# Kernel optimization log

Measured on AMD Instinct MI355X. Metric: run time of the kernel, lower is better.

The kernel has to match this reference:

```python
import jax, jax.numpy as jnp
import numpy as np

N_CARD, N_TX, N_MER = 100_000, 1_000_000, 10_000
E = 1_000_000
H = 128


def setup_inputs() -> dict:
    key = jax.random.key(0)
    ks = iter(jax.random.split(key, 32))
    nrm = lambda shape, s=1.0: jax.random.normal(next(ks), shape, jnp.float32) * s
    W = 0.05  # weight scale for numerical sanity across two relu layers
    inp = {
        "x_card": nrm((N_CARD, 32)),
        "x_tx": nrm((N_TX, 64)),
        "x_mer": nrm((N_MER, 32)),
        # layer-1 SAGEConv params per edge type: lin_l (src->H, w/ bias), lin_r (dst->H)
        "l1_pays_wl": nrm((32, H), W), "l1_pays_bl": nrm((H,), W), "l1_pays_wr": nrm((64, H), W),
        "l1_recv_wl": nrm((32, H), W), "l1_recv_bl": nrm((H,), W), "l1_recv_wr": nrm((64, H), W),
        "l1_rpays_wl": nrm((64, H), W), "l1_rpays_bl": nrm((H,), W), "l1_rpays_wr": nrm((32, H), W),
        "l1_rrecv_wl": nrm((64, H), W), "l1_rrecv_bl": nrm((H,), W), "l1_rrecv_wr": nrm((32, H), W),
        # layer-2: all relations are H->H; stacked in order [pays, receives, rev_pays, rev_receives]
        "w2l": nrm((4, H, H), W), "b2": nrm((4, H), W), "w2r": nrm((4, H, H), W),
        # final lazy Linear(-1, out_channels=1) -> (H, 1)
        "wf": nrm((H, 1), W), "bf": nrm((1,), W),
        "pays_src": jax.random.randint(next(ks), (E,), 0, N_CARD, jnp.int32),
        "pays_dst": jnp.arange(E, dtype=jnp.int32),
        "recv_src": jax.random.randint(next(ks), (E,), 0, N_MER, jnp.int32),
        "recv_dst": jnp.arange(E, dtype=jnp.int32),
    }
    return inp


def _sage(x_src, x_dst, src, dst, wl, bl, wr, n_dst):
    """PyG SAGEConv(aggr='mean'): lin_l(mean_j x_j) + lin_r(x_root)."""
    msg = x_src[src]  # [E, d_src] gather
    s = jax.ops.segment_sum(msg, dst, num_segments=n_dst)
    cnt = jax.ops.segment_sum(jnp.ones((src.shape[0], 1), msg.dtype), dst, num_segments=n_dst)
    mean = s / jnp.maximum(cnt, 1.0)
    return mean @ wl + bl + x_dst @ wr


def reference(x_card, x_tx, x_mer,
              l1_pays_wl, l1_pays_bl, l1_pays_wr,
              l1_recv_wl, l1_recv_bl, l1_recv_wr,
              l1_rpays_wl, l1_rpays_bl, l1_rpays_wr,
              l1_rrecv_wl, l1_rrecv_bl, l1_rrecv_wr,
              w2l, b2, w2r, wf, bf,
              pays_src, pays_dst, recv_src, recv_dst):
    # ---- layer 1 (HeteroConv aggr='sum' over relations sharing a dst type) ----
    tx = (_sage(x_card, x_tx, pays_src, pays_dst, l1_pays_wl, l1_pays_bl, l1_pays_wr, N_TX)
          + _sage(x_mer, x_tx, recv_src, recv_dst, l1_recv_wl, l1_recv_bl, l1_recv_wr, N_TX))
    # rev_pays / rev_receives are the transposed edge lists
    card = _sage(x_tx, x_card, pays_dst, pays_src, l1_rpays_wl, l1_rpays_bl, l1_rpays_wr, N_CARD)
    mer = _sage(x_tx, x_mer, recv_dst, recv_src, l1_rrecv_wl, l1_rrecv_bl, l1_rrecv_wr, N_MER)
    tx, card, mer = jax.nn.relu(tx), jax.nn.relu(card), jax.nn.relu(mer)
    # ---- layer 2 (only transaction output feeds the head; card/mer layer-2 outputs unused) ----
    tx2 = (_sage(card, tx, pays_src, pays_dst, w2l[0], b2[0], w2r[0], N_TX)
           + _sage(mer, tx, recv_src, recv_dst, w2l[1], b2[1], w2r[1], N_TX))
    tx2 = jax.nn.relu(tx2)
    return tx2 @ wf + bf  # [N_TX, 1]
```

## Files before the change

### kernel.cpp

```cpp
#include <hip/hip_runtime.h>
#include <hip/hip_bf16.h>
#include <stdint.h>

#define NCARD 100000
#define NTX   1000000
#define NMER  10000
#define NE    1000000
#define CAPC  48
#define CAPM  192
#define NCB   3125
#define NMB   313


typedef __attribute__((ext_vector_type(8))) short bf16x8;
typedef __attribute__((ext_vector_type(4))) float f32x4;

__device__ inline unsigned short f2bf(float f) {
  union { float f; uint32_t u; } v; v.f = f;
  uint32_t r = v.u + 0x7FFF + ((v.u >> 16) & 1);
  return (unsigned short)(r >> 16);
}
__device__ inline float bf2f(unsigned short u) {
  union { uint32_t u; float f; } v; v.u = ((uint32_t)u) << 16;
  return v.f;
}
__device__ inline uint32_t addpack2(uint32_t a, uint32_t b) {
  float lo = bf2f((unsigned short)(a & 0xffff)) + bf2f((unsigned short)(b & 0xffff));
  float hi = bf2f((unsigned short)(a >> 16))   + bf2f((unsigned short)(b >> 16));
  return (uint32_t)f2bf(lo) | ((uint32_t)f2bf(hi) << 16);
}

#define OFF_WR1T  0u
#define OFF_W2RT  4096u
#define OFF_B1    12288u
#define OFF_B2    12416u
#define OFF_CW1   12544u
#define OFF_CW2   18688u
#define OFF_CW3   26880u
#define OFF_MW1   28928u
#define OFF_MW2   35072u
#define OFF_MW3   43264u
#define OFF_CQ    45312u
#define OFF_MQ    12845312u
#define OFF_CCNT  14125312u
#define OFF_MCNT  14225312u
#define OFF_CBUK  14235312u
#define OFF_MBUK  19035312u
#define OFF_XB    20955312u
#define WS_END    52955312u

__global__ __launch_bounds__(256) void k_prep_all(
    const float* __restrict__ pays_wr, const float* __restrict__ recv_wr,
    const float* __restrict__ w2r, const float* __restrict__ pays_bl,
    const float* __restrict__ recv_bl, const float* __restrict__ b2,
    unsigned short* __restrict__ wr1t, unsigned short* __restrict__ w2rt,
    float* __restrict__ b1sum, float* __restrict__ b2sum,
    const float* __restrict__ c_wl64, const float* __restrict__ c_wr32,
    const float* __restrict__ c_w2, const float* __restrict__ c_wg,
    unsigned short* __restrict__ cw1, unsigned short* __restrict__ cw2,
    unsigned short* __restrict__ cw3,
    const float* __restrict__ m_wl64, const float* __restrict__ m_wr32,
    const float* __restrict__ m_w2, const float* __restrict__ m_wg,
    unsigned short* __restrict__ mw1, unsigned short* __restrict__ mw2,
    unsigned short* __restrict__ mw3)
{
  const int grp = blockIdx.x >> 6;
  const int i = (blockIdx.x & 63) * 256 + threadIdx.x;
  if (grp == 0) {
    if (i < 8192) {
      int n = i >> 6, k = i & 63;
      wr1t[i] = f2bf(pays_wr[k * 128 + n] + recv_wr[k * 128 + n]);
    }
    if (i < 16384) {
      int n = i >> 7, k = i & 127;
      w2rt[i] = f2bf(w2r[k * 128 + n] + w2r[16384 + k * 128 + n]);
    }
    if (i < 128) {
      b1sum[i] = pays_bl[i] + recv_bl[i];
      b2sum[i] = b2[i] + b2[128 + i];
    }
  } else {
    const float* wl64 = (grp == 1) ? c_wl64 : m_wl64;
    const float* wr32 = (grp == 1) ? c_wr32 : m_wr32;
    const float* w2   = (grp == 1) ? c_w2   : m_w2;
    const float* wg   = (grp == 1) ? c_wg   : m_wg;
    unsigned short* w1t = (grp == 1) ? cw1 : mw1;
    unsigned short* w2t = (grp == 1) ? cw2 : mw2;
    unsigned short* w3t = (grp == 1) ? cw3 : mw3;
    if (i < 12288) {
      int n = i / 96, k = i % 96;
      float v = (k < 64) ? wl64[k * 128 + n] : wr32[(k - 64) * 128 + n];
      w1t[i] = f2bf(v);
    }
    if (i < 16384) { int n = i >> 7, k = i & 127; w2t[i] = f2bf(w2[k * 128 + n]); }
    if (i < 4096)  { int n = i >> 5, k = i & 31;  w3t[i] = f2bf(wg[k * 128 + n]); }
  }
}

__global__ __launch_bounds__(256) void k_convert_build(
    const float* __restrict__ x, unsigned short* __restrict__ xb,
    const int* __restrict__ ps, const int* __restrict__ rs,
    int* __restrict__ ccnt, int* __restrict__ mcnt,
    int* __restrict__ cbuk, int* __restrict__ mbuk)
{
  int64_t i = (int64_t)blockIdx.x * 256 + threadIdx.x;
  if (i < 16000000) {
    float4 v = ((const float4*)x)[i];
    unsigned short p[4] = { f2bf(v.x), f2bf(v.y), f2bf(v.z), f2bf(v.w) };
    *(uint2*)&xb[i * 4] = *(const uint2*)p;
  }
  if (i < NE) {
    int e = (int)i;
    int c = ps[e];
    int pos = atomicAdd(ccnt + c, 1);
    if (pos < CAPC) cbuk[c * CAPC + pos] = e;
    int m = rs[e];
    int pm = atomicAdd(mcnt + m, 1);
    if (pm < CAPM) mbuk[m * CAPM + pm] = e;
  }
}

__global__ __launch_bounds__(256) void k_node_both(
    const int* __restrict__ ccnt, const int* __restrict__ cbuk,
    const int* __restrict__ mcnt, const int* __restrict__ mbuk,
    const unsigned short* __restrict__ xb,
    const float* __restrict__ x_card, const float* __restrict__ x_mer,
    const unsigned short* __restrict__ cw1, const unsigned short* __restrict__ cw2,
    const unsigned short* __restrict__ cw3, const float* __restrict__ cbl,
    const unsigned short* __restrict__ mw1, const unsigned short* __restrict__ mw2,
    const unsigned short* __restrict__ mw3, const float* __restrict__ mbl,
    const float* __restrict__ b1sum, const float* __restrict__ b2sum,
    unsigned short* __restrict__ cq, unsigned short* __restrict__ mq)
{
  const bool iscard = blockIdx.x < NCB;
  const int* cnt = iscard ? ccnt : mcnt;
  const int* buk = iscard ? cbuk : mbuk;
  const int cap  = iscard ? CAPC : CAPM;
  const int R    = iscard ? NCARD : NMER;
  const float* x_node = iscard ? x_card : x_mer;
  const unsigned short* w1t = iscard ? cw1 : mw1;
  const unsigned short* w2t = iscard ? cw2 : mw2;
  const unsigned short* w3t = iscard ? cw3 : mw3;
  const float* bl = iscard ? cbl : mbl;
  unsigned short* q = iscard ? cq : mq;
  const int n0 = (iscard ? blockIdx.x : blockIdx.x - NCB) * 32;

  __shared__ unsigned short ms[32 * 64];
  __shared__ unsigned short xs2[32 * 32];
  __shared__ unsigned short ts[32 * 128];
  __shared__ float bll[128], ba1[128], ba2[128];
  const int tid = threadIdx.x;
  const int wv = tid >> 6, l = tid & 63;
  const int lr = l & 15, lk = l >> 4;

  bf16x8 f1[2][3], f2w[2][4], f3[2];
#pragma unroll
  for (int c = 0; c < 2; ++c) {
    const int n = wv * 32 + c * 16 + lr;
#pragma unroll
    for (int k = 0; k < 3; ++k)
      f1[c][k] = *(const bf16x8*)(w1t + n * 96 + k * 32 + lk * 8);
#pragma unroll
    for (int k = 0; k < 4; ++k)
      f2w[c][k] = *(const bf16x8*)(w2t + n * 128 + k * 32 + lk * 8);
    f3[c] = *(const bf16x8*)(w3t + n * 32 + lk * 8);
  }
  if (tid < 128) {
    bll[tid] = bl[tid];
    ba1[tid] = iscard ? b1sum[tid] : 0.f;
    ba2[tid] = iscard ? b2sum[tid] : 0.f;
  }

  const int half = l >> 5, c32 = l & 31;
  for (int rr = wv; rr < 32; rr += 4) {
    const int node = n0 + rr;
    int deg = 0;
    if (node < R) deg = cnt[node];
    const int64_t base = (int64_t)node * cap;
    float a0 = 0.f, a1 = 0.f;
    int p = half;
    for (; p + 14 < deg; p += 16) {
      int ei[8];
      uint32_t vi[8];
#pragma unroll
      for (int u = 0; u < 8; ++u) ei[u] = buk[base + p + 2 * u];
#pragma unroll
      for (int u = 0; u < 8; ++u)
        vi[u] = *(const uint32_t*)&xb[(int64_t)ei[u] * 64 + c32 * 2];
#pragma unroll
      for (int u = 0; u < 8; ++u) {
        a0 += bf2f((unsigned short)(vi[u] & 0xffff));
        a1 += bf2f((unsigned short)(vi[u] >> 16));
      }
    }
    for (; p + 6 < deg; p += 8) {
      int e0 = buk[base + p],     e1 = buk[base + p + 2];
      int e2 = buk[base + p + 4], e3 = buk[base + p + 6];
      uint32_t v0 = *(const uint32_t*)&xb[(int64_t)e0 * 64 + c32 * 2];
      uint32_t v1 = *(const uint32_t*)&xb[(int64_t)e1 * 64 + c32 * 2];
      uint32_t v2 = *(const uint32_t*)&xb[(int64_t)e2 * 64 + c32 * 2];
      uint32_t v3 = *(const uint32_t*)&xb[(int64_t)e3 * 64 + c32 * 2];
      a0 += bf2f((unsigned short)(v0 & 0xffff)) + bf2f((unsigned short)(v1 & 0xffff))
          + bf2f((unsigned short)(v2 & 0xffff)) + bf2f((unsigned short)(v3 & 0xffff));
      a1 += bf2f((unsigned short)(v0 >> 16)) + bf2f((unsigned short)(v1 >> 16))
          + bf2f((unsigned short)(v2 >> 16)) + bf2f((unsigned short)(v3 >> 16));
    }
    for (; p < deg; p += 2) {
      int e = buk[base + p];
      uint32_t v = *(const uint32_t*)&xb[(int64_t)e * 64 + c32 * 2];
      a0 += bf2f((unsigned short)(v & 0xffff));
      a1 += bf2f((unsigned short)(v >> 16));
    }
    a0 += __shfl_xor(a0, 32, 64);
    a1 += __shfl_xor(a1, 32, 64);
    if (half == 0) {
      float inv = 1.f / fmaxf((float)deg, 1.f);
      unsigned short pr[2] = { f2bf(a0 * inv), f2bf(a1 * inv) };
      int li = (rr * 64 + c32 * 2) ^ ((rr & 7) << 3);
      *(uint32_t*)&ms[li] = *(const uint32_t*)pr;
    }
  }
#pragma unroll
  for (int q4 = 0; q4 < 4; ++q4) {
    int id = q4 * 256 + tid;
    int r = id >> 5, c = id & 31;
    float v = (n0 + r < R) ? x_node[(int64_t)(n0 + r) * 32 + c] : 0.f;
    xs2[(r * 32 + c) ^ ((r & 3) << 3)] = f2bf(v);
  }
  __syncthreads();

#pragma unroll
  for (int rt = 0; rt < 2; ++rt) {
    const int arow = rt * 16 + lr;
    const int sw = (arow & 7) << 3, sw2 = (arow & 3) << 3;
    bf16x8 a0 = *(const bf16x8*)&ms[(arow * 64 + 0  + lk * 8) ^ sw];
    bf16x8 a1 = *(const bf16x8*)&ms[(arow * 64 + 32 + lk * 8) ^ sw];
    bf16x8 ax = *(const bf16x8*)&xs2[(arow * 32 + lk * 8) ^ sw2];
    f32x4 acc0 = {0.f,0.f,0.f,0.f}, acc1 = {0.f,0.f,0.f,0.f};
    acc0 = __builtin_amdgcn_mfma_f32_16x16x32_bf16(a0, f1[0][0], acc0, 0, 0, 0);
    acc0 = __builtin_amdgcn_mfma_f32_16x16x32_bf16(a1, f1[0][1], acc0, 0, 0, 0);
    acc0 = __builtin_amdgcn_mfma_f32_16x16x32_bf16(ax, f1[0][2], acc0, 0, 0, 0);
    acc1 = __builtin_amdgcn_mfma_f32_16x16x32_bf16(a0, f1[1][0], acc1, 0, 0, 0);
    acc1 = __builtin_amdgcn_mfma_f32_16x16x32_bf16(a1, f1[1][1], acc1, 0, 0, 0);
    acc1 = __builtin_amdgcn_mfma_f32_16x16x32_bf16(ax, f1[1][2], acc1, 0, 0, 0);
#pragma unroll
    for (int c = 0; c < 2; ++c) {
      const int col = wv * 32 + c * 16 + lr;
#pragma unroll
      for (int i = 0; i < 4; ++i) {
        const int r = rt * 16 + lk * 4 + i;
        float v = (c ? acc1[i] : acc0[i]) + bll[col];
        ts[(r * 128 + col) ^ ((r & 7) << 3)] = f2bf(fmaxf(v, 0.f));
      }
    }
  }
  __syncthreads();

#pragma unroll
  for (int rt = 0; rt < 2; ++rt) {
    const int arow = rt * 16 + lr;
    const int sw = (arow & 7) << 3, sw2 = (arow & 3) << 3;
    f32x4 b0 = {0.f,0.f,0.f,0.f}, b1a = {0.f,0.f,0.f,0.f};
#pragma unroll
    for (int kk = 0; kk < 4; ++kk) {
      bf16x8 a = *(const bf16x8*)&ts[(arow * 128 + kk * 32 + lk * 8) ^ sw];
      b0  = __builtin_amdgcn_mfma_f32_16x16x32_bf16(a, f2w[0][kk], b0, 0, 0, 0);
      b1a = __builtin_amdgcn_mfma_f32_16x16x32_bf16(a, f2w[1][kk], b1a, 0, 0, 0);
    }
    bf16x8 ax = *(const bf16x8*)&xs2[(arow * 32 + lk * 8) ^ sw2];
    f32x4 g0 = {0.f,0.f,0.f,0.f}, g1a = {0.f,0.f,0.f,0.f};
    g0  = __builtin_amdgcn_mfma_f32_16x16x32_bf16(ax, f3[0], g0, 0, 0, 0);
    g1a = __builtin_amdgcn_mfma_f32_16x16x32_bf16(ax, f3[1], g1a, 0, 0, 0);
#pragma unroll
    for (int c = 0; c < 2; ++c) {
#pragma unroll
      for (int i = 0; i < 4; ++i) {
        const int node = n0 + rt * 16 + lk * 4 + i;
        const int col = wv * 32 + c * 16 + lr;
        if (node < R) {
          q[node * 256 + col]       = f2bf((c ? g1a[i] : g0[i]) + ba1[col]);
          q[node * 256 + 128 + col] = f2bf((c ? b1a[i] : b0[i]) + ba2[col]);
        }
      }
    }
  }
}

#define TXR 32
__global__ __launch_bounds__(256) void k_fused_tx_mfma(
    const unsigned short* __restrict__ xb,
    const int* __restrict__ ps, const int* __restrict__ rs,
    const unsigned short* __restrict__ cq, const unsigned short* __restrict__ mq,
    const unsigned short* __restrict__ wr1t, const unsigned short* __restrict__ w2rt,
    const float* __restrict__ wf, const float* __restrict__ bfp,
    float* __restrict__ out)
{
  __shared__ unsigned short xs[TXR * 64];
  __shared__ unsigned short ts[TXR * 128];
  __shared__ unsigned short g1[TXR * 128];
  __shared__ unsigned short g2[TXR * 128];
  __shared__ float partial[4][TXR];
  __shared__ float wfl[128];

  const int tid = threadIdx.x;
  const int wv = tid >> 6;
  const int l  = tid & 63;
  const int lr = l & 15;
  const int lk = l >> 4;

  bf16x8 w1f[2][2], w2f[2][4];
#pragma unroll
  for (int c = 0; c < 2; ++c) {
    const int n = (wv * 2 + c) * 16 + lr;
#pragma unroll
    for (int kk = 0; kk < 2; ++kk)
      w1f[c][kk] = *(const bf16x8*)(wr1t + n * 64 + kk * 32 + lk * 8);
#pragma unroll
    for (int kk = 0; kk < 4; ++kk)
      w2f[c][kk] = *(const bf16x8*)(w2rt + n * 128 + kk * 32 + lk * 8);
  }
  if (tid < 128) wfl[tid] = wf[tid];
  const float bfv = bfp[0];

  const uint32_t* cqd = (const uint32_t*)cq;
  const uint32_t* mqd = (const uint32_t*)mq;

  const int r_x = tid >> 3, seg_x = tid & 7;
  const int64_t stride = (int64_t)gridDim.x * TXR;
  int64_t row0 = (int64_t)blockIdx.x * TXR;

  uint4 xv;
  uint32_t rc1[8], rm1[8], rc2[8], rm2[8];

  if (row0 < NTX) {
    xv = *(const uint4*)&xb[(row0 + r_x) * 64 + seg_x * 8];
#pragma unroll
    for (int p = 0; p < 8; ++p) {
      const int r = p * 4 + wv;
      const int64_t c = ps[row0 + r];
      const int64_t m = rs[row0 + r];
      rc1[p] = cqd[c * 128 + l];      rm1[p] = mqd[m * 128 + l];
      rc2[p] = cqd[c * 128 + 64 + l]; rm2[p] = mqd[m * 128 + 64 + l];
    }
  }

  for (; row0 < NTX; row0 += stride) {
    __syncthreads();
    *(uint4*)&xs[(r_x * 64 + seg_x * 8) ^ ((r_x & 7) << 3)] = xv;
#pragma unroll
    for (int p = 0; p < 8; ++p) {
      const int r = p * 4 + wv;
      const int dst = r * 64 + (l ^ (p << 3));
      ((uint32_t*)g1)[dst] = addpack2(rc1[p], rm1[p]);
      ((uint32_t*)g2)[dst] = addpack2(rc2[p], rm2[p]);
    }
    __syncthreads();

    const int64_t nxt = row0 + stride;
    if (nxt < NTX) {
      xv = *(const uint4*)&xb[(nxt + r_x) * 64 + seg_x * 8];
#pragma unroll
      for (int p = 0; p < 8; ++p) {
        const int r = p * 4 + wv;
        const int64_t c = ps[nxt + r];
        const int64_t m = rs[nxt + r];
        rc1[p] = cqd[c * 128 + l];      rm1[p] = mqd[m * 128 + l];
        rc2[p] = cqd[c * 128 + 64 + l]; rm2[p] = mqd[m * 128 + 64 + l];
      }
    }

#pragma unroll
    for (int rt = 0; rt < 2; ++rt) {
      const int arow = rt * 16 + lr;
      const int sw = (arow & 7) << 3;
      bf16x8 a0  = *(const bf16x8*)&xs[(arow * 64 + 0  + lk * 8) ^ sw];
      bf16x8 a1v = *(const bf16x8*)&xs[(arow * 64 + 32 + lk * 8) ^ sw];
      f32x4 acc0 = {0.f,0.f,0.f,0.f}, acc1 = {0.f,0.f,0.f,0.f};
      acc0 = __builtin_amdgcn_mfma_f32_16x16x32_bf16(a0,  w1f[0][0], acc0, 0, 0, 0);
      acc0 = __builtin_amdgcn_mfma_f32_16x16x32_bf16(a1v, w1f[0][1], acc0, 0, 0, 0);
      acc1 = __builtin_amdgcn_mfma_f32_16x16x32_bf16(a0,  w1f[1][0], acc1, 0, 0, 0);
      acc1 = __builtin_amdgcn_mfma_f32_16x16x32_bf16(a1v, w1f[1][1], acc1, 0, 0, 0);
      const int gx = (rt * 4 + lk) << 3;
#pragma unroll
      for (int c = 0; c < 2; ++c) {
        const int col = wv * 32 + c * 16 + lr;
        const int gofs = (((col >> 1) ^ gx) << 1) + (col & 1);
        const f32x4 acc = c ? acc1 : acc0;
#pragma unroll
        for (int i = 0; i < 4; ++i) {
          const int r = rt * 16 + lk * 4 + i;
          float v = acc[i] + bf2f(g1[r * 128 + gofs]);
          ts[(r * 128 + col) ^ ((r & 7) << 3)] = f2bf(fmaxf(v, 0.f));
        }
      }
    }
    __syncthreads();

#pragma unroll
    for (int rt = 0; rt < 2; ++rt) {
      const int arow = rt * 16 + lr;
      const int sw = (arow & 7) << 3;
      f32x4 acc0 = {0.f,0.f,0.f,0.f}, acc1 = {0.f,0.f,0.f,0.f};
#pragma unroll
      for (int kk = 0; kk < 4; ++kk) {
        bf16x8 a = *(const bf16x8*)&ts[(arow * 128 + kk * 32 + lk * 8) ^ sw];
        acc0 = __builtin_amdgcn_mfma_f32_16x16x32_bf16(a, w2f[0][kk], acc0, 0, 0, 0);
        acc1 = __builtin_amdgcn_mfma_f32_16x16x32_bf16(a, w2f[1][kk], acc1, 0, 0, 0);
      }
      const int gx = (rt * 4 + lk) << 3;
#pragma unroll
      for (int i = 0; i < 4; ++i) {
        const int r = rt * 16 + lk * 4 + i;
        float sum = 0.f;
#pragma unroll
        for (int c = 0; c < 2; ++c) {
          const int col = wv * 32 + c * 16 + lr;
          const int gofs = (((col >> 1) ^ gx) << 1) + (col & 1);
          float y = (c ? acc1[i] : acc0[i]) + bf2f(g2[r * 128 + gofs]);
          sum = fmaf(fmaxf(y, 0.f), wfl[col], sum);
        }
#pragma unroll
        for (int off = 1; off < 16; off <<= 1) sum += __shfl_xor(sum, off, 64);
        if (lr == 0) partial[wv][r] = sum;
      }
    }
    __syncthreads();
    if (tid < TXR)
      out[row0 + tid] = partial[0][tid] + partial[1][tid] + partial[2][tid]
                      + partial[3][tid] + bfv;
  }
}

extern "C" void kernel_launch(void* const* d_in, const int* in_sizes, int n_in,
                              void* d_out, int out_size, void* d_ws, size_t ws_size,
                              hipStream_t stream) {
  const float* x_card = (const float*)d_in[0];
  const float* x_tx   = (const float*)d_in[1];
  const float* x_mer  = (const float*)d_in[2];
  const float* l1_pays_wl = (const float*)d_in[3];
  const float* l1_pays_bl = (const float*)d_in[4];
  const float* l1_pays_wr = (const float*)d_in[5];
  const float* l1_recv_wl = (const float*)d_in[6];
  const float* l1_recv_bl = (const float*)d_in[7];
  const float* l1_recv_wr = (const float*)d_in[8];
  const float* l1_rpays_wl = (const float*)d_in[9];
  const float* l1_rpays_bl = (const float*)d_in[10];
  const float* l1_rpays_wr = (const float*)d_in[11];
  const float* l1_rrecv_wl = (const float*)d_in[12];
  const float* l1_rrecv_bl = (const float*)d_in[13];
  const float* l1_rrecv_wr = (const float*)d_in[14];
  const float* w2l = (const float*)d_in[15];
  const float* b2  = (const float*)d_in[16];
  const float* w2r = (const float*)d_in[17];
  const float* wf  = (const float*)d_in[18];
  const float* bf  = (const float*)d_in[19];
  const int* pays_src = (const int*)d_in[20];
  const int* recv_src = (const int*)d_in[22];

  float* ws = (float*)d_ws;
  unsigned short* wr1t = (unsigned short*)(ws + OFF_WR1T);
  unsigned short* w2rt = (unsigned short*)(ws + OFF_W2RT);
  float* b1sum = ws + OFF_B1;
  float* b2sum = ws + OFF_B2;
  unsigned short* cw1 = (unsigned short*)(ws + OFF_CW1);
  unsigned short* cw2 = (unsigned short*)(ws + OFF_CW2);
  unsigned short* cw3 = (unsigned short*)(ws + OFF_CW3);
  unsigned short* mw1 = (unsigned short*)(ws + OFF_MW1);
  unsigned short* mw2 = (unsigned short*)(ws + OFF_MW2);
  unsigned short* mw3 = (unsigned short*)(ws + OFF_MW3);
  unsigned short* cq  = (unsigned short*)(ws + OFF_CQ);
  unsigned short* mq  = (unsigned short*)(ws + OFF_MQ);
  int* ccnt = (int*)(ws + OFF_CCNT);
  int* mcnt = (int*)(ws + OFF_MCNT);
  int* cbuk = (int*)(ws + OFF_CBUK);
  int* mbuk = (int*)(ws + OFF_MBUK);
  unsigned short* xb = (unsigned short*)(ws + OFF_XB);

  hipMemsetAsync((char*)d_ws + (size_t)OFF_CCNT * 4, 0,
                 (size_t)(OFF_CBUK - OFF_CCNT) * 4, stream);

  k_prep_all<<<192, 256, 0, stream>>>(
      l1_pays_wr, l1_recv_wr, w2r, l1_pays_bl, l1_recv_bl, b2,
      wr1t, w2rt, b1sum, b2sum,
      l1_rpays_wl, l1_rpays_wr, w2l, l1_pays_wl, cw1, cw2, cw3,
      l1_rrecv_wl, l1_rrecv_wr, w2l + 16384, l1_recv_wl, mw1, mw2, mw3);

  k_convert_build<<<62500, 256, 0, stream>>>(x_tx, xb, pays_src, recv_src,
                                             ccnt, mcnt, cbuk, mbuk);

  k_node_both<<<NCB + NMB, 256, 0, stream>>>(
      ccnt, cbuk, mcnt, mbuk, xb, x_card, x_mer,
      cw1, cw2, cw3, l1_rpays_bl,
      mw1, mw2, mw3, l1_rrecv_bl,
      b1sum, b2sum, cq, mq);

  k_fused_tx_mfma<<<2048, 256, 0, stream>>>(xb, pays_src, recv_src, cq, mq,
                                            wr1t, w2rt, wf, bf, (float*)d_out);
}
```

Before: 649.5 us.

## Drop bf16 staging copy of x_tx and read fp32 directly in consumers

Removes the pass that converted all of x_tx (256 MB fp32) to a bf16 buffer, so the build kernel only bucketizes edges. The node-aggregation kernel now gathers fp32 pairs straight from x_tx, and the fused tx kernel loads fp32 with nontemporal loads and converts to bf16 when writing to LDS. The output store also becomes nontemporal. This saves one full read plus a half-size write of x_tx, but the card and merchant gathers and the tx streaming now move twice the bytes per element compared with the bf16 copy.

```diff
diff --git a/kernel.cpp b/kernel.cpp
--- a/kernel.cpp
+++ b/kernel.cpp
@@ -14,6 +14,8 @@
 
 typedef __attribute__((ext_vector_type(8))) short bf16x8;
 typedef __attribute__((ext_vector_type(4))) float f32x4;
+typedef __attribute__((ext_vector_type(4))) float f32x4v;
+typedef __attribute__((ext_vector_type(2))) float f32x2v;
 
 __device__ inline unsigned short f2bf(float f) {
   union { float f; uint32_t u; } v; v.f = f;
@@ -46,8 +48,7 @@
 #define OFF_MCNT  14225312u
 #define OFF_CBUK  14235312u
 #define OFF_MBUK  19035312u
-#define OFF_XB    20955312u
-#define WS_END    52955312u
+#define WS_END    20955312u
 
 __global__ __launch_bounds__(256) void k_prep_all(
     const float* __restrict__ pays_wr, const float* __restrict__ recv_wr,
@@ -97,20 +98,13 @@
   }
 }
 
-__global__ __launch_bounds__(256) void k_convert_build(
-    const float* __restrict__ x, unsigned short* __restrict__ xb,
+__global__ __launch_bounds__(256) void k_build(
     const int* __restrict__ ps, const int* __restrict__ rs,
     int* __restrict__ ccnt, int* __restrict__ mcnt,
     int* __restrict__ cbuk, int* __restrict__ mbuk)
 {
-  int64_t i = (int64_t)blockIdx.x * 256 + threadIdx.x;
-  if (i < 16000000) {
-    float4 v = ((const float4*)x)[i];
-    unsigned short p[4] = { f2bf(v.x), f2bf(v.y), f2bf(v.z), f2bf(v.w) };
-    *(uint2*)&xb[i * 4] = *(const uint2*)p;
-  }
-  if (i < NE) {
-    int e = (int)i;
+  int e = blockIdx.x * 256 + threadIdx.x;
+  if (e < NE) {
     int c = ps[e];
     int pos = atomicAdd(ccnt + c, 1);
     if (pos < CAPC) cbuk[c * CAPC + pos] = e;
@@ -123,7 +117,7 @@
 __global__ __launch_bounds__(256) void k_node_both(
     const int* __restrict__ ccnt, const int* __restrict__ cbuk,
     const int* __restrict__ mcnt, const int* __restrict__ mbuk,
-    const unsigned short* __restrict__ xb,
+    const float* __restrict__ xtx,
     const float* __restrict__ x_card, const float* __restrict__ x_mer,
     const unsigned short* __restrict__ cw1, const unsigned short* __restrict__ cw2,
     const unsigned short* __restrict__ cw3, const float* __restrict__ cbl,
@@ -181,35 +175,28 @@
     int p = half;
     for (; p + 14 < deg; p += 16) {
       int ei[8];
-      uint32_t vi[8];
+      f32x2v vi[8];
 #pragma unroll
       for (int u = 0; u < 8; ++u) ei[u] = buk[base + p + 2 * u];
 #pragma unroll
       for (int u = 0; u < 8; ++u)
-        vi[u] = *(const uint32_t*)&xb[(int64_t)ei[u] * 64 + c32 * 2];
-#pragma unroll
-      for (int u = 0; u < 8; ++u) {
-        a0 += bf2f((unsigned short)(vi[u] & 0xffff));
-        a1 += bf2f((unsigned short)(vi[u] >> 16));
-      }
+        vi[u] = *(const f32x2v*)&xtx[(int64_t)ei[u] * 64 + c32 * 2];
+#pragma unroll
+      for (int u = 0; u < 8; ++u) { a0 += vi[u].x; a1 += vi[u].y; }
     }
     for (; p + 6 < deg; p += 8) {
       int e0 = buk[base + p],     e1 = buk[base + p + 2];
       int e2 = buk[base + p + 4], e3 = buk[base + p + 6];
-      uint32_t v0 = *(const uint32_t*)&xb[(int64_t)e0 * 64 + c32 * 2];
-      uint32_t v1 = *(const uint32_t*)&xb[(int64_t)e1 * 64 + c32 * 2];
-      uint32_t v2 = *(const uint32_t*)&xb[(int64_t)e2 * 64 + c32 * 2];
-      uint32_t v3 = *(const uint32_t*)&xb[(int64_t)e3 * 64 + c32 * 2];
-      a0 += bf2f((unsigned short)(v0 & 0xffff)) + bf2f((unsigned short)(v1 & 0xffff))
-          + bf2f((unsigned short)(v2 & 0xffff)) + bf2f((unsigned short)(v3 & 0xffff));
-      a1 += bf2f((unsigned short)(v0 >> 16)) + bf2f((unsigned short)(v1 >> 16))
-          + bf2f((unsigned short)(v2 >> 16)) + bf2f((unsigned short)(v3 >> 16));
+      f32x2v v0 = *(const f32x2v*)&xtx[(int64_t)e0 * 64 + c32 * 2];
+      f32x2v v1 = *(const f32x2v*)&xtx[(int64_t)e1 * 64 + c32 * 2];
+      f32x2v v2 = *(const f32x2v*)&xtx[(int64_t)e2 * 64 + c32 * 2];
+      f32x2v v3 = *(const f32x2v*)&xtx[(int64_t)e3 * 64 + c32 * 2];
+      a0 += v0.x + v1.x + v2.x + v3.x;
+      a1 += v0.y + v1.y + v2.y + v3.y;
     }
     for (; p < deg; p += 2) {
-      int e = buk[base + p];
-      uint32_t v = *(const uint32_t*)&xb[(int64_t)e * 64 + c32 * 2];
-      a0 += bf2f((unsigned short)(v & 0xffff));
-      a1 += bf2f((unsigned short)(v >> 16));
+      f32x2v v = *(const f32x2v*)&xtx[(int64_t)buk[base + p] * 64 + c32 * 2];
+      a0 += v.x; a1 += v.y;
     }
     a0 += __shfl_xor(a0, 32, 64);
     a1 += __shfl_xor(a1, 32, 64);
@@ -288,7 +275,7 @@
 
 #define TXR 32
 __global__ __launch_bounds__(256) void k_fused_tx_mfma(
-    const unsigned short* __restrict__ xb,
+    const float* __restrict__ xtx,
     const int* __restrict__ ps, const int* __restrict__ rs,
     const unsigned short* __restrict__ cq, const unsigned short* __restrict__ mq,
     const unsigned short* __restrict__ wr1t, const unsigned short* __restrict__ w2rt,
@@ -329,11 +316,13 @@
   const int64_t stride = (int64_t)gridDim.x * TXR;
   int64_t row0 = (int64_t)blockIdx.x * TXR;
 
-  uint4 xv;
+  f32x4v xva, xvb;
   uint32_t rc1[8], rm1[8], rc2[8], rm2[8];
 
   if (row0 < NTX) {
-    xv = *(const uint4*)&xb[(row0 + r_x) * 64 + seg_x * 8];
+    const float* xp = &xtx[(row0 + r_x) * 64 + seg_x * 8];
+    xva = __builtin_nontemporal_load((const f32x4v*)xp);
+    xvb = __builtin_nontemporal_load((const f32x4v*)(xp + 4));
 #pragma unroll
     for (int p = 0; p < 8; ++p) {
       const int r = p * 4 + wv;
@@ -346,7 +335,11 @@
 
   for (; row0 < NTX; row0 += stride) {
     __syncthreads();
-    *(uint4*)&xs[(r_x * 64 + seg_x * 8) ^ ((r_x & 7) << 3)] = xv;
+    {
+      unsigned short p8[8] = { f2bf(xva.x), f2bf(xva.y), f2bf(xva.z), f2bf(xva.w),
+                               f2bf(xvb.x), f2bf(xvb.y), f2bf(xvb.z), f2bf(xvb.w) };
+      *(uint4*)&xs[(r_x * 64 + seg_x * 8) ^ ((r_x & 7) << 3)] = *(const uint4*)p8;
+    }
 #pragma unroll
     for (int p = 0; p < 8; ++p) {
       const int r = p * 4 + wv;
@@ -358,7 +351,9 @@
 
     const int64_t nxt = row0 + stride;
     if (nxt < NTX) {
-      xv = *(const uint4*)&xb[(nxt + r_x) * 64 + seg_x * 8];
+      const float* xp = &xtx[(nxt + r_x) * 64 + seg_x * 8];
+      xva = __builtin_nontemporal_load((const f32x4v*)xp);
+      xvb = __builtin_nontemporal_load((const f32x4v*)(xp + 4));
 #pragma unroll
       for (int p = 0; p < 8; ++p) {
         const int r = p * 4 + wv;
@@ -425,9 +420,11 @@
       }
     }
     __syncthreads();
-    if (tid < TXR)
-      out[row0 + tid] = partial[0][tid] + partial[1][tid] + partial[2][tid]
-                      + partial[3][tid] + bfv;
+    if (tid < TXR) {
+      float o = partial[0][tid] + partial[1][tid] + partial[2][tid]
+              + partial[3][tid] + bfv;
+      __builtin_nontemporal_store(o, &out[row0 + tid]);
+    }
   }
 }
 
@@ -474,7 +471,6 @@
   int* mcnt = (int*)(ws + OFF_MCNT);
   int* cbuk = (int*)(ws + OFF_CBUK);
   int* mbuk = (int*)(ws + OFF_MBUK);
-  unsigned short* xb = (unsigned short*)(ws + OFF_XB);
 
   hipMemsetAsync((char*)d_ws + (size_t)OFF_CCNT * 4, 0,
                  (size_t)(OFF_CBUK - OFF_CCNT) * 4, stream);
@@ -485,15 +481,15 @@
       l1_rpays_wl, l1_rpays_wr, w2l, l1_pays_wl, cw1, cw2, cw3,
       l1_rrecv_wl, l1_rrecv_wr, w2l + 16384, l1_recv_wl, mw1, mw2, mw3);
 
-  k_convert_build<<<62500, 256, 0, stream>>>(x_tx, xb, pays_src, recv_src,
-                                             ccnt, mcnt, cbuk, mbuk);
+  k_build<<<(NE + 255) / 256, 256, 0, stream>>>(pays_src, recv_src,
+                                                ccnt, mcnt, cbuk, mbuk);
 
   k_node_both<<<NCB + NMB, 256, 0, stream>>>(
-      ccnt, cbuk, mcnt, mbuk, xb, x_card, x_mer,
+      ccnt, cbuk, mcnt, mbuk, x_tx, x_card, x_mer,
       cw1, cw2, cw3, l1_rpays_bl,
       mw1, mw2, mw3, l1_rrecv_bl,
       b1sum, b2sum, cq, mq);
 
-  k_fused_tx_mfma<<<2048, 256, 0, stream>>>(xb, pays_src, recv_src, cq, mq,
+  k_fused_tx_mfma<<<2048, 256, 0, stream>>>(x_tx, pays_src, recv_src, cq, mq,
                                             wr1t, w2rt, wf, bf, (float*)d_out);
 }
```

Result: slower. 670.9 us (+3.3%).

## Drop register prefetch in fused tx kernel to raise occupancy, share gather buffer

Applied to the files above, without the earlier changes.

Removes the software-pipelined register prefetch of the next tile's gathered card/merchant rows and x rows, replacing it with in-loop gathers and direct global loads of x for the MFMA A operand. The two gather LDS buffers are merged into one reused buffer, filled in two phases with an extra barrier, and launch bounds request 5 blocks per SM. The aim is to cut register and LDS pressure so more waves can hide gather latency. The cost is giving up explicit overlap of the next tile's loads with compute, plus an added sync.

```diff
diff --git a/kernel.cpp b/kernel.cpp
--- a/kernel.cpp
+++ b/kernel.cpp
@@ -287,7 +287,7 @@
 }
 
 #define TXR 32
-__global__ __launch_bounds__(256) void k_fused_tx_mfma(
+__global__ __launch_bounds__(256, 5) void k_fused_tx_mfma(
     const unsigned short* __restrict__ xb,
     const int* __restrict__ ps, const int* __restrict__ rs,
     const unsigned short* __restrict__ cq, const unsigned short* __restrict__ mq,
@@ -295,10 +295,8 @@
     const float* __restrict__ wf, const float* __restrict__ bfp,
     float* __restrict__ out)
 {
-  __shared__ unsigned short xs[TXR * 64];
+  __shared__ unsigned short gs[TXR * 128];
   __shared__ unsigned short ts[TXR * 128];
-  __shared__ unsigned short g1[TXR * 128];
-  __shared__ unsigned short g2[TXR * 128];
   __shared__ float partial[4][TXR];
   __shared__ float wfl[128];
 
@@ -325,56 +323,24 @@
   const uint32_t* cqd = (const uint32_t*)cq;
   const uint32_t* mqd = (const uint32_t*)mq;
 
-  const int r_x = tid >> 3, seg_x = tid & 7;
   const int64_t stride = (int64_t)gridDim.x * TXR;
-  int64_t row0 = (int64_t)blockIdx.x * TXR;
-
-  uint4 xv;
-  uint32_t rc1[8], rm1[8], rc2[8], rm2[8];
-
-  if (row0 < NTX) {
-    xv = *(const uint4*)&xb[(row0 + r_x) * 64 + seg_x * 8];
+
+  for (int64_t row0 = (int64_t)blockIdx.x * TXR; row0 < NTX; row0 += stride) {
 #pragma unroll
     for (int p = 0; p < 8; ++p) {
       const int r = p * 4 + wv;
       const int64_t c = ps[row0 + r];
       const int64_t m = rs[row0 + r];
-      rc1[p] = cqd[c * 128 + l];      rm1[p] = mqd[m * 128 + l];
-      rc2[p] = cqd[c * 128 + 64 + l]; rm2[p] = mqd[m * 128 + 64 + l];
-    }
-  }
-
-  for (; row0 < NTX; row0 += stride) {
+      const int dst = r * 64 + (l ^ (p << 3));
+      ((uint32_t*)gs)[dst] = addpack2(cqd[c * 128 + l], mqd[m * 128 + l]);
+    }
     __syncthreads();
-    *(uint4*)&xs[(r_x * 64 + seg_x * 8) ^ ((r_x & 7) << 3)] = xv;
-#pragma unroll
-    for (int p = 0; p < 8; ++p) {
-      const int r = p * 4 + wv;
-      const int dst = r * 64 + (l ^ (p << 3));
-      ((uint32_t*)g1)[dst] = addpack2(rc1[p], rm1[p]);
-      ((uint32_t*)g2)[dst] = addpack2(rc2[p], rm2[p]);
-    }
-    __syncthreads();
-
-    const int64_t nxt = row0 + stride;
-    if (nxt < NTX) {
-      xv = *(const uint4*)&xb[(nxt + r_x) * 64 + seg_x * 8];
-#pragma unroll
-      for (int p = 0; p < 8; ++p) {
-        const int r = p * 4 + wv;
-        const int64_t c = ps[nxt + r];
-        const int64_t m = rs[nxt + r];
-        rc1[p] = cqd[c * 128 + l];      rm1[p] = mqd[m * 128 + l];
-        rc2[p] = cqd[c * 128 + 64 + l]; rm2[p] = mqd[m * 128 + 64 + l];
-      }
-    }
 
 #pragma unroll
     for (int rt = 0; rt < 2; ++rt) {
       const int arow = rt * 16 + lr;
-      const int sw = (arow & 7) << 3;
-      bf16x8 a0  = *(const bf16x8*)&xs[(arow * 64 + 0  + lk * 8) ^ sw];
-      bf16x8 a1v = *(const bf16x8*)&xs[(arow * 64 + 32 + lk * 8) ^ sw];
+      const bf16x8 a0  = *(const bf16x8*)&xb[(row0 + arow) * 64 + lk * 8];
+      const bf16x8 a1v = *(const bf16x8*)&xb[(row0 + arow) * 64 + 32 + lk * 8];
       f32x4 acc0 = {0.f,0.f,0.f,0.f}, acc1 = {0.f,0.f,0.f,0.f};
       acc0 = __builtin_amdgcn_mfma_f32_16x16x32_bf16(a0,  w1f[0][0], acc0, 0, 0, 0);
       acc0 = __builtin_amdgcn_mfma_f32_16x16x32_bf16(a1v, w1f[0][1], acc0, 0, 0, 0);
@@ -389,10 +355,20 @@
 #pragma unroll
         for (int i = 0; i < 4; ++i) {
           const int r = rt * 16 + lk * 4 + i;
-          float v = acc[i] + bf2f(g1[r * 128 + gofs]);
+          float v = acc[i] + bf2f(gs[r * 128 + gofs]);
           ts[(r * 128 + col) ^ ((r & 7) << 3)] = f2bf(fmaxf(v, 0.f));
         }
       }
+    }
+    __syncthreads();
+
+#pragma unroll
+    for (int p = 0; p < 8; ++p) {
+      const int r = p * 4 + wv;
+      const int64_t c = ps[row0 + r];
+      const int64_t m = rs[row0 + r];
+      const int dst = r * 64 + (l ^ (p << 3));
+      ((uint32_t*)gs)[dst] = addpack2(cqd[c * 128 + 64 + l], mqd[m * 128 + 64 + l]);
     }
     __syncthreads();
 
@@ -416,7 +392,7 @@
         for (int c = 0; c < 2; ++c) {
           const int col = wv * 32 + c * 16 + lr;
           const int gofs = (((col >> 1) ^ gx) << 1) + (col & 1);
-          float y = (c ? acc1[i] : acc0[i]) + bf2f(g2[r * 128 + gofs]);
+          float y = (c ? acc1[i] : acc0[i]) + bf2f(gs[r * 128 + gofs]);
           sum = fmaf(fmaxf(y, 0.f), wfl[col], sum);
         }
 #pragma unroll
@@ -476,8 +452,8 @@
   int* mbuk = (int*)(ws + OFF_MBUK);
   unsigned short* xb = (unsigned short*)(ws + OFF_XB);
 
-  hipMemsetAsync((char*)d_ws + (size_t)OFF_CCNT * 4, 0,
-                 (size_t)(OFF_CBUK - OFF_CCNT) * 4, stream);
+  (void)hipMemsetAsync((char*)d_ws + (size_t)OFF_CCNT * 4, 0,
+                       (size_t)(OFF_CBUK - OFF_CCNT) * 4, stream);
 
   k_prep_all<<<192, 256, 0, stream>>>(
       l1_pays_wr, l1_recv_wr, w2r, l1_pays_bl, l1_recv_bl, b2,
```

Result: slower. 1.224 ms (+88.5%).
